# Kernel tuning notes

Measured on AMD Instinct MI355X. Metric: run time of the kernel, lower is better.

## Reference

```python
import jax, jax.numpy as jnp
import numpy as np

B, S, H, D, E = 1, 2048, 16, 64, 1024
STRIDE, LCMP = 16, 32          # compression stride / block
LSEL, TOPN = 64, 16            # selection block size / top-k blocks
WIN = 512                      # sliding window
NEG = jnp.float32(-1e9)


def setup_inputs() -> dict:
    key = jax.random.key(0)
    ks = jax.random.split(key, 5)
    q = jax.random.normal(ks[0], (B, S, H, D), jnp.float32)
    k = jax.random.normal(ks[1], (B, S, H, D), jnp.float32)
    v = jax.random.normal(ks[2], (B, S, H, D), jnp.float32)
    x = jax.random.normal(ks[3], (B, S, E), jnp.float32)
    Wg = jax.random.normal(ks[4], (E, 3), jnp.float32) * 0.02
    bg = jnp.zeros((3,), jnp.float32)
    cu_seqlens = jnp.array([0, S], jnp.int32)
    max_seqlen = S
    return {"q": q, "k": k, "v": v, "x": x, "Wg": Wg, "bg": bg,
            "cu_seqlens": cu_seqlens, "max_seqlen": max_seqlen}


def _nsa_forward(q, k, v, x, Wg, bg):
    scale = 1.0 / np.sqrt(D)
    t = jnp.arange(S)
    num_cmp = (S - LCMP) // STRIDE + 1   # 127
    num_sel = S // LSEL                  # 32

    # ---- branch 1: compressed-KV attention (mean-pooled blocks) ----
    starts = jnp.arange(num_cmp) * STRIDE
    widx = starts[:, None] + jnp.arange(LCMP)          # (num_cmp, LCMP)
    Kc = k[:, widx].mean(axis=2)                        # (B, num_cmp, H, D)
    Vc = v[:, widx].mean(axis=2)
    logits_c = jnp.einsum('bshd,bchd->bhsc', q, Kc) * scale
    # query t may attend only to fully-past compressed blocks
    mask_c = (starts + LCMP)[None, :] <= (t[:, None] + 1)   # (S, num_cmp)
    p_c = jax.nn.softmax(jnp.where(mask_c[None, None], logits_c, NEG), axis=-1)
    valid_c = mask_c.any(axis=-1).astype(q.dtype)           # (S,) zero-out empty rows
    p_c = p_c * valid_c[None, None, :, None]
    o_cmp = jnp.einsum('bhsc,bchd->bshd', p_c, Vc)

    # ---- branch 2: top-k selected-block attention ----
    # map compressed-block scores -> selection-block importance (overlap sum)
    sel_s = jnp.arange(num_sel) * LSEL
    overlap = ((starts[:, None] < sel_s[None, :] + LSEL) &
               (starts[:, None] + LCMP > sel_s[None, :])).astype(q.dtype)  # (num_cmp, num_sel)
    p_sel = jnp.einsum('bhsc,cn->bhsn', p_c, overlap)        # (B,H,S,num_sel)
    _, top_idx = jax.lax.top_k(p_sel, TOPN)                  # (B,H,S,TOPN)
    sel_blk = jax.nn.one_hot(top_idx, num_sel).sum(axis=-2) > 0   # (B,H,S,num_sel)
    own_blk = jax.nn.one_hot(t // LSEL, num_sel) > 0              # always include own block
    sel_blk = sel_blk | own_blk[None, None]
    sel_tok = jnp.repeat(sel_blk, LSEL, axis=-1)             # (B,H,S,S) token-level mask

    causal = t[:, None] >= t[None, :]                        # (S,S)
    logits = jnp.einsum('bshd,bthd->bhst', q, k) * scale     # (B,H,S,S), shared by 2 branches
    a_sel = jax.nn.softmax(jnp.where(sel_tok & causal[None, None], logits, NEG), axis=-1)
    o_sel = jnp.einsum('bhst,bthd->bshd', a_sel, v)

    # ---- branch 3: sliding-window attention ----
    win_mask = causal & (t[:, None] - t[None, :] < WIN)
    a_win = jax.nn.softmax(jnp.where(win_mask[None, None], logits, NEG), axis=-1)
    o_win = jnp.einsum('bhst,bthd->bshd', a_win, v)

    # ---- learned gating over the 3 branches ----
    g = jax.nn.sigmoid(x @ Wg + bg)                          # (B,S,3)
    out = (g[..., 0][..., None, None] * o_cmp +
           g[..., 1][..., None, None] * o_sel +
           g[..., 2][..., None, None] * o_win)
    return out                                               # (B,S,H,D)


def reference(q, k, v, x, Wg, bg, cu_seqlens, max_seqlen):
    return _nsa_forward(q, k, v, x, Wg, bg)
```

## Files before the change

### kernel.cpp

```cpp
#include <hip/hip_runtime.h>
#include <hip/hip_bf16.h>
#include <math.h>

#define H_NUM 16
#define D_DIM 64
#define S_LEN 2048
#define E_DIM 1024
#define NC    127
#define TOPN  16
#define SCALE 0.125f

typedef short s16x8 __attribute__((ext_vector_type(8)));
typedef short s16x4 __attribute__((ext_vector_type(4)));
typedef float f32x4 __attribute__((ext_vector_type(4)));
typedef unsigned short ushort_t;

__device__ __forceinline__ unsigned short f2b(float f) {
    __hip_bfloat16 h = __float2bfloat16(f);
    return *reinterpret_cast<unsigned short*>(&h);
}
__device__ __forceinline__ float b2f(unsigned short u) {
    __hip_bfloat16 h = *reinterpret_cast<__hip_bfloat16*>(&u);
    return __bfloat162float(h);
}
__device__ __forceinline__ s16x8 pack8(float4 a, float4 b) {
    s16x8 r;
    r[0] = (short)f2b(a.x); r[1] = (short)f2b(a.y);
    r[2] = (short)f2b(a.z); r[3] = (short)f2b(a.w);
    r[4] = (short)f2b(b.x); r[5] = (short)f2b(b.y);
    r[6] = (short)f2b(b.z); r[7] = (short)f2b(b.w);
    return r;
}
__device__ __forceinline__ f32x4 mfma16(s16x8 a, s16x8 b, f32x4 c) {
    return __builtin_amdgcn_mfma_f32_16x16x32_bf16(a, b, c, 0, 0, 0);
}
__device__ __forceinline__ void wave_lds_fence() {
    asm volatile("s_waitcnt lgkmcnt(0)" ::: "memory");
    __builtin_amdgcn_sched_barrier(0);
}
__device__ __forceinline__ int swP(int r, int c) { return r * 128 + (c ^ ((r & 7) << 2)); }
__device__ __forceinline__ int swB(int r, int c) { return r * 128 + (c ^ ((r & 7) << 3)); }

__device__ __forceinline__ float wave_sum(float v) {
#pragma unroll
    for (int off = 32; off; off >>= 1) v += __shfl_xor(v, off, 64);
    return v;
}

__global__ __launch_bounds__(64) void nsa_compress(
    const float* __restrict__ k, const float* __restrict__ v,
    ushort_t* __restrict__ KcHi, ushort_t* __restrict__ KcLo, ushort_t* __restrict__ VcT)
{
    int bid = blockIdx.x;
    int h = bid >> 7, c = bid & 127;
    int lane = threadIdx.x;
    float mk = 0.f, mv = 0.f;
    if (c < NC) {
        int s0 = c * 16;
#pragma unroll 4
        for (int i = 0; i < 32; ++i) {
            mk += k[((size_t)(s0 + i) * H_NUM + h) * D_DIM + lane];
            mv += v[((size_t)(s0 + i) * H_NUM + h) * D_DIM + lane];
        }
        mk *= (1.f / 32.f); mv *= (1.f / 32.f);
    }
    unsigned short khi = f2b(mk);
    KcHi[((size_t)h * 128 + c) * 64 + lane] = khi;
    KcLo[((size_t)h * 128 + c) * 64 + lane] = f2b(mk - b2f(khi));
    VcT[((size_t)h * 64 + lane) * 128 + c] = f2b(mv);
}

__global__ __launch_bounds__(256) void nsa_cast_k(
    const float* __restrict__ k, ushort_t* __restrict__ Kb)
{
    int idx = (blockIdx.x * 256 + threadIdx.x) * 4;
    int d = idx & 63, s = (idx >> 6) & 2047, h = idx >> 17;
    float4 f = *(const float4*)(k + ((size_t)s * H_NUM + h) * D_DIM + d);
    s16x4 u;
    u[0] = (short)f2b(f.x); u[1] = (short)f2b(f.y);
    u[2] = (short)f2b(f.z); u[3] = (short)f2b(f.w);
    *(s16x4*)(Kb + idx) = u;
}

__global__ __launch_bounds__(256) void nsa_cast_vt(
    const float* __restrict__ v, ushort_t* __restrict__ VtB)
{
    __shared__ ushort_t T[64][136];
    int h = blockIdx.x >> 4, s0 = (blockIdx.x & 15) << 7;
    int tid = threadIdx.x;
#pragma unroll
    for (int rep = 0; rep < 8; ++rep) {
        int idx = rep * 256 + tid;
        int i = idx >> 4, d4 = (idx & 15) << 2;
        float4 f = *(const float4*)(v + ((size_t)(s0 + i) * H_NUM + h) * D_DIM + d4);
        T[d4 + 0][i] = f2b(f.x); T[d4 + 1][i] = f2b(f.y);
        T[d4 + 2][i] = f2b(f.z); T[d4 + 3][i] = f2b(f.w);
    }
    __syncthreads();
    int d = tid >> 2, i0 = (tid & 3) << 5;
    ushort_t* dst = VtB + ((size_t)h * 64 + d) * 2048 + s0 + i0;
#pragma unroll
    for (int jj = 0; jj < 32; jj += 8)
        *(s16x8*)(dst + jj) = *(const s16x8*)&T[d][i0 + jj];
}

__global__ __launch_bounds__(64) void nsa_gate(
    const float* __restrict__ x, const float* __restrict__ Wg,
    const float* __restrict__ bg, float* __restrict__ g)
{
    int s = blockIdx.x, lane = threadIdx.x;
    float a0 = 0.f, a1 = 0.f, a2 = 0.f;
    for (int i = lane; i < E_DIM; i += 64) {
        float xv = x[(size_t)s * E_DIM + i];
        a0 = fmaf(xv, Wg[i * 3 + 0], a0);
        a1 = fmaf(xv, Wg[i * 3 + 1], a1);
        a2 = fmaf(xv, Wg[i * 3 + 2], a2);
    }
    a0 = wave_sum(a0); a1 = wave_sum(a1); a2 = wave_sum(a2);
    if (lane == 0) {
        g[s * 3 + 0] = 1.f / (1.f + expf(-(a0 + bg[0])));
        g[s * 3 + 1] = 1.f / (1.f + expf(-(a1 + bg[1])));
        g[s * 3 + 2] = 1.f / (1.f + expf(-(a2 + bg[2])));
    }
}

__global__ __launch_bounds__(256) void nsa_main(
    const float* __restrict__ q,
    const ushort_t* __restrict__ Kb, const ushort_t* __restrict__ VtB,
    const ushort_t* __restrict__ KcHi, const ushort_t* __restrict__ KcLo,
    const ushort_t* __restrict__ VcT,
    const float* __restrict__ gat, float* __restrict__ out)
{
    __shared__ __align__(16) float Pl[4 * 2048];
    __shared__ __align__(16) float psl[4 * 512];

    const int bid  = blockIdx.x;
    const int h    = bid & 15;
    const int grp  = bid >> 4;
    const int tile = (grp < 16) ? (31 - grp) : (grp - 16);
    const int t0   = tile << 6;
    const int tid  = threadIdx.x;
    const int w    = tid >> 6;
    const int lane = tid & 63;
    const int lr   = lane & 15;
    const int g    = lane >> 4;

    float*    Pw   = Pl + w * 2048;
    ushort_t* Pb   = (ushort_t*)Pw;
    float*    pslw = psl + w * 512;

    int trow[4];
#pragma unroll
    for (int r = 0; r < 4; ++r) trow[r] = t0 + 16 * w + 4 * g + r;

    s16x8 qa[2], ql[2];
    {
        const float* qrow = q + ((size_t)(t0 + 16 * w + lr) * H_NUM + h) * D_DIM;
#pragma unroll
        for (int kk = 0; kk < 2; ++kk) {
            float4 a = *(const float4*)(qrow + kk * 32 + g * 8);
            float4 b = *(const float4*)(qrow + kk * 32 + g * 8 + 4);
            s16x8 hi = pack8(a, b);
            float4 ar, br;
            ar.x = a.x - b2f((unsigned short)hi[0]); ar.y = a.y - b2f((unsigned short)hi[1]);
            ar.z = a.z - b2f((unsigned short)hi[2]); ar.w = a.w - b2f((unsigned short)hi[3]);
            br.x = b.x - b2f((unsigned short)hi[4]); br.y = b.y - b2f((unsigned short)hi[5]);
            br.z = b.z - b2f((unsigned short)hi[6]); br.w = b.w - b2f((unsigned short)hi[7]);
            qa[kk] = hi;
            ql[kk] = pack8(ar, br);
        }
    }

    f32x4 sc8[8];
#pragma unroll
    for (int ct = 0; ct < 8; ++ct) {
        f32x4 acc = {0.f, 0.f, 0.f, 0.f};
#pragma unroll
        for (int kk = 0; kk < 2; ++kk) {
            const size_t off = ((size_t)h * 128 + 16 * ct + lr) * 64 + kk * 32 + g * 8;
            s16x8 khi = *(const s16x8*)(KcHi + off);
            s16x8 klo = *(const s16x8*)(KcLo + off);
            acc = mfma16(qa[kk], khi, acc);
            acc = mfma16(ql[kk], khi, acc);
            acc = mfma16(qa[kk], klo, acc);
        }
        sc8[ct] = acc;
    }

    int nv[4];
#pragma unroll
    for (int r = 0; r < 4; ++r) nv[r] = (trow[r] >= 31) ? (((trow[r] - 31) >> 4) + 1) : 0;

    float pm[4] = {-3e38f, -3e38f, -3e38f, -3e38f};
#pragma unroll
    for (int ct = 0; ct < 8; ++ct)
#pragma unroll
        for (int r = 0; r < 4; ++r) {
            int c = 16 * ct + lr;
            float s = sc8[ct][r] * SCALE;
            if (c < nv[r]) pm[r] = fmaxf(pm[r], s);
        }
#pragma unroll
    for (int off = 8; off >= 1; off >>= 1)
#pragma unroll
        for (int r = 0; r < 4; ++r) pm[r] = fmaxf(pm[r], __shfl_xor(pm[r], off, 64));

    float l1[4] = {0.f, 0.f, 0.f, 0.f};
#pragma unroll
    for (int ct = 0; ct < 8; ++ct)
#pragma unroll
        for (int r = 0; r < 4; ++r) {
            int c = 16 * ct + lr;
            float p = (c < nv[r]) ? __expf(sc8[ct][r] * SCALE - pm[r]) : 0.f;
            l1[r] += p;
            Pw[swP(4 * g + r, 16 * ct + lr)] = p;
        }
#pragma unroll
    for (int off = 8; off >= 1; off >>= 1)
#pragma unroll
        for (int r = 0; r < 4; ++r) l1[r] += __shfl_xor(l1[r], off, 64);
    wave_lds_fence();

#pragma unroll
    for (int rep = 0; rep < 8; ++rep) {
        int item = rep * 64 + lane;
        int n = item >> 4, row = item & 15;
        int lo = 4 * n - 1; if (lo < 0) lo = 0;
        int hi = 4 * n + 3; if (hi > NC - 1) hi = NC - 1;
        float s = 0.f;
        for (int c = lo; c <= hi; ++c) s += Pw[swP(row, c)];
        pslw[n * 16 + row] = s;
    }
    wave_lds_fence();

    unsigned mymask = 0u;
    {
        float pv[32];
#pragma unroll
        for (int n = 0; n < 32; ++n) pv[n] = (lane < 16) ? pslw[n * 16 + lane] : 0.f;
        for (int it = 0; it < TOPN; ++it) {
            float best = -1.f; int bi = 0;
#pragma unroll
            for (int n = 0; n < 32; ++n) {
                float val = ((mymask >> n) & 1u) ? -2.f : pv[n];
                if (val > best) { best = val; bi = n; }
            }
            mymask |= 1u << bi;
        }
        mymask |= 1u << tile;
        if (lane >= 16) mymask = 0u;
    }
    unsigned um = mymask;
#pragma unroll
    for (int off = 32; off >= 1; off >>= 1) um |= __shfl_xor(um, off, 64);
    unsigned selreg[4];
#pragma unroll
    for (int r = 0; r < 4; ++r) selreg[r] = __shfl(mymask, 4 * g + r, 64);

    f32x4 oc[4];
#pragma unroll
    for (int dt = 0; dt < 4; ++dt) { f32x4 z = {0.f, 0.f, 0.f, 0.f}; oc[dt] = z; }
#pragma unroll
    for (int kk = 0; kk < 4; ++kk) {
        float4 a0 = *(const float4*)&Pw[swP(lr, kk * 32 + g * 8)];
        float4 a1 = *(const float4*)&Pw[swP(lr, kk * 32 + g * 8 + 4)];
        s16x8 pa = pack8(a0, a1);
#pragma unroll
        for (int dt = 0; dt < 4; ++dt)
            oc[dt] = mfma16(pa, *(const s16x8*)(VcT + ((size_t)h * 64 + 16 * dt + lr) * 128 + kk * 32 + g * 8), oc[dt]);
    }

    const int winlo = (tile >= 8) ? (tile - 8) : 0;

    float m2[4], l2[4], m3[4], l3[4];
    f32x4 o2[4], o3[4];
#pragma unroll
    for (int r = 0; r < 4; ++r) { m2[r] = -1e30f; l2[r] = 0.f; m3[r] = -1e30f; l3[r] = 0.f; }
#pragma unroll
    for (int dt = 0; dt < 4; ++dt) { f32x4 z = {0.f, 0.f, 0.f, 0.f}; o2[dt] = z; o3[dt] = z; }

    for (int n = 0; n <= tile; ++n) {
        const bool sel_on = (um >> n) & 1u;
        const bool win_on = n >= winlo;
        if (!sel_on && !win_on) continue;
        const int base = n << 6;

        f32x4 s4[4];
#pragma unroll
        for (int ct = 0; ct < 4; ++ct) {
            f32x4 acc = {0.f, 0.f, 0.f, 0.f};
#pragma unroll
            for (int kk = 0; kk < 2; ++kk)
                acc = mfma16(qa[kk],
                    *(const s16x8*)(Kb + ((size_t)h * 2048 + base + 16 * ct + lr) * 64 + kk * 32 + g * 8), acc);
            s4[ct] = acc;
        }

        if (sel_on) {
            float rm[4] = {-3e38f, -3e38f, -3e38f, -3e38f};
#pragma unroll
            for (int ct = 0; ct < 4; ++ct)
#pragma unroll
                for (int r = 0; r < 4; ++r) {
                    int j = base + 16 * ct + lr;
                    bool ok = ((selreg[r] >> n) & 1u) && (j <= trow[r]);
                    float s = s4[ct][r] * SCALE;
                    if (ok) rm[r] = fmaxf(rm[r], s);
                }
#pragma unroll
            for (int off = 8; off >= 1; off >>= 1)
#pragma unroll
                for (int r = 0; r < 4; ++r) rm[r] = fmaxf(rm[r], __shfl_xor(rm[r], off, 64));
            float al[4], rs[4] = {0.f, 0.f, 0.f, 0.f};
#pragma unroll
            for (int r = 0; r < 4; ++r) {
                float mn = fmaxf(m2[r], rm[r]);
                al[r] = __expf(m2[r] - mn);
                m2[r] = mn;
            }
#pragma unroll
            for (int ct = 0; ct < 4; ++ct)
#pragma unroll
                for (int r = 0; r < 4; ++r) {
                    int j = base + 16 * ct + lr;
                    bool ok = ((selreg[r] >> n) & 1u) && (j <= trow[r]);
                    float p = ok ? __expf(s4[ct][r] * SCALE - m2[r]) : 0.f;
                    rs[r] += p;
                    Pb[swB(4 * g + r, 16 * ct + lr)] = f2b(p);
                }
#pragma unroll
            for (int off = 8; off >= 1; off >>= 1)
#pragma unroll
                for (int r = 0; r < 4; ++r) rs[r] += __shfl_xor(rs[r], off, 64);
#pragma unroll
            for (int r = 0; r < 4; ++r) l2[r] = l2[r] * al[r] + rs[r];
#pragma unroll
            for (int dt = 0; dt < 4; ++dt)
#pragma unroll
                for (int r = 0; r < 4; ++r) o2[dt][r] *= al[r];
        }
        if (win_on) {
            float rm[4] = {-3e38f, -3e38f, -3e38f, -3e38f};
#pragma unroll
            for (int ct = 0; ct < 4; ++ct)
#pragma unroll
                for (int r = 0; r < 4; ++r) {
                    int j = base + 16 * ct + lr;
                    bool ok = (j >= trow[r] - 511) && (j <= trow[r]);
                    float s = s4[ct][r] * SCALE;
                    if (ok) rm[r] = fmaxf(rm[r], s);
                }
#pragma unroll
            for (int off = 8; off >= 1; off >>= 1)
#pragma unroll
                for (int r = 0; r < 4; ++r) rm[r] = fmaxf(rm[r], __shfl_xor(rm[r], off, 64));
            float al[4], rs[4] = {0.f, 0.f, 0.f, 0.f};
#pragma unroll
            for (int r = 0; r < 4; ++r) {
                float mn = fmaxf(m3[r], rm[r]);
                al[r] = __expf(m3[r] - mn);
                m3[r] = mn;
            }
#pragma unroll
            for (int ct = 0; ct < 4; ++ct)
#pragma unroll
                for (int r = 0; r < 4; ++r) {
                    int j = base + 16 * ct + lr;
                    bool ok = (j >= trow[r] - 511) && (j <= trow[r]);
                    float p = ok ? __expf(s4[ct][r] * SCALE - m3[r]) : 0.f;
                    rs[r] += p;
                    Pb[2048 + swB(4 * g + r, 16 * ct + lr)] = f2b(p);
                }
#pragma unroll
            for (int off = 8; off >= 1; off >>= 1)
#pragma unroll
                for (int r = 0; r < 4; ++r) rs[r] += __shfl_xor(rs[r], off, 64);
#pragma unroll
            for (int r = 0; r < 4; ++r) l3[r] = l3[r] * al[r] + rs[r];
#pragma unroll
            for (int dt = 0; dt < 4; ++dt)
#pragma unroll
                for (int r = 0; r < 4; ++r) o3[dt][r] *= al[r];
        }
        wave_lds_fence();

        if (sel_on) {
#pragma unroll
            for (int kk = 0; kk < 2; ++kk) {
                s16x8 pa = *(const s16x8*)&Pb[swB(lr, kk * 32 + g * 8)];
#pragma unroll
                for (int dt = 0; dt < 4; ++dt)
                    o2[dt] = mfma16(pa,
                        *(const s16x8*)(VtB + ((size_t)h * 64 + 16 * dt + lr) * 2048 + base + kk * 32 + g * 8), o2[dt]);
            }
        }
        if (win_on) {
#pragma unroll
            for (int kk = 0; kk < 2; ++kk) {
                s16x8 pa = *(const s16x8*)&Pb[2048 + swB(lr, kk * 32 + g * 8)];
#pragma unroll
                for (int dt = 0; dt < 4; ++dt)
                    o3[dt] = mfma16(pa,
                        *(const s16x8*)(VtB + ((size_t)h * 64 + 16 * dt + lr) * 2048 + base + kk * 32 + g * 8), o3[dt]);
            }
        }
    }

#pragma unroll
    for (int r = 0; r < 4; ++r) {
        const float* gp = gat + (size_t)trow[r] * 3;
        float g0 = gp[0], g1 = gp[1], g2 = gp[2];
        float invc = nv[r] ? (1.f / l1[r]) : 0.f;
        float i2 = 1.f / l2[r], i3 = 1.f / l3[r];
#pragma unroll
        for (int dt = 0; dt < 4; ++dt) {
            float val = g0 * (oc[dt][r] * invc) + g1 * (o2[dt][r] * i2) + g2 * (o3[dt][r] * i3);
            out[((size_t)trow[r] * H_NUM + h) * D_DIM + 16 * dt + lr] = val;
        }
    }
}

extern "C" void kernel_launch(void* const* d_in, const int* in_sizes, int n_in,
                              void* d_out, int out_size, void* d_ws, size_t ws_size,
                              hipStream_t stream) {
    const float* q  = (const float*)d_in[0];
    const float* k  = (const float*)d_in[1];
    const float* v  = (const float*)d_in[2];
    const float* x  = (const float*)d_in[3];
    const float* Wg = (const float*)d_in[4];
    const float* bg = (const float*)d_in[5];
    float* out = (float*)d_out;

    ushort_t* Kb   = (ushort_t*)d_ws;
    ushort_t* VtB  = Kb  + (size_t)16 * 2048 * 64;
    ushort_t* KcHi = VtB + (size_t)16 * 64 * 2048;
    ushort_t* KcLo = KcHi + (size_t)16 * 128 * 64;
    ushort_t* VcT  = KcLo + (size_t)16 * 128 * 64;
    float*    g    = (float*)(VcT + (size_t)16 * 64 * 128);

    nsa_compress<<<16 * 128, 64, 0, stream>>>(k, v, KcHi, KcLo, VcT);
    nsa_cast_k  <<<2048, 256, 0, stream>>>(k, Kb);
    nsa_cast_vt <<<256, 256, 0, stream>>>(v, VtB);
    nsa_gate    <<<S_LEN, 64, 0, stream>>>(x, Wg, bg, g);
    nsa_main    <<<512, 256, 0, stream>>>(q, Kb, VtB, KcHi, KcLo, VcT, g, out);
}
```

Measured before the change: 152.3 us.

## Split attention branches across paired waves with 512-thread blocks and merge results

Doubles the block to 8 waves and pairs each 16-row group across two waves. One wave computes the compressed branch and top-k selection while its partner runs the sliding-window loop. Both waves then share the selected-block loop by alternating blocks, and the partial online-softmax states are merged through shared memory. This aims to shorten the serial per-wave critical path and raise the number of resident waves, at the cost of extra LDS, two block-wide barriers and a merge step.

```diff
diff --git a/kernel.cpp b/kernel.cpp
--- a/kernel.cpp
+++ b/kernel.cpp
@@ -39,7 +39,7 @@
     __builtin_amdgcn_sched_barrier(0);
 }
 __device__ __forceinline__ int swP(int r, int c) { return r * 128 + (c ^ ((r & 7) << 2)); }
-__device__ __forceinline__ int swB(int r, int c) { return r * 128 + (c ^ ((r & 7) << 3)); }
+__device__ __forceinline__ int swU(int r, int c) { return r * 64  + (c ^ ((r & 7) << 3)); }
 
 __device__ __forceinline__ float wave_sum(float v) {
 #pragma unroll
@@ -124,15 +124,18 @@
     }
 }
 
-__global__ __launch_bounds__(256) void nsa_main(
+__global__ __launch_bounds__(512, 4) void nsa_main(
     const float* __restrict__ q,
     const ushort_t* __restrict__ Kb, const ushort_t* __restrict__ VtB,
     const ushort_t* __restrict__ KcHi, const ushort_t* __restrict__ KcLo,
     const ushort_t* __restrict__ VcT,
     const float* __restrict__ gat, float* __restrict__ out)
 {
-    __shared__ __align__(16) float Pl[4 * 2048];
-    __shared__ __align__(16) float psl[4 * 512];
+    __shared__ __align__(16) float    P1[4 * 2048];
+    __shared__ __align__(16) float    psl[4 * 512];
+    __shared__ __align__(16) ushort_t BP[4 * 2048];
+    __shared__ float    mrg[4 * 64];
+    __shared__ unsigned selm_l[64];
 
     const int bid  = blockIdx.x;
     const int h    = bid & 15;
@@ -141,21 +144,26 @@
     const int t0   = tile << 6;
     const int tid  = threadIdx.x;
     const int w    = tid >> 6;
+    const int pair = w & 3;
+    const bool isA = w < 4;
     const int lane = tid & 63;
     const int lr   = lane & 15;
     const int g    = lane >> 4;
-
-    float*    Pw   = Pl + w * 2048;
-    ushort_t* Pb   = (ushort_t*)Pw;
-    float*    pslw = psl + w * 512;
+    const int rb   = t0 + 16 * pair;
+
+    float*    P1w  = P1 + pair * 2048;
+    float*    pslw = psl + pair * 512;
+    ushort_t* APb  = (ushort_t*)pslw;
+    ushort_t* BPw  = BP + pair * 2048;
+    float*    mrgw = mrg + pair * 64;
 
     int trow[4];
 #pragma unroll
-    for (int r = 0; r < 4; ++r) trow[r] = t0 + 16 * w + 4 * g + r;
+    for (int r = 0; r < 4; ++r) trow[r] = rb + 4 * g + r;
 
     s16x8 qa[2], ql[2];
     {
-        const float* qrow = q + ((size_t)(t0 + 16 * w + lr) * H_NUM + h) * D_DIM;
+        const float* qrow = q + ((size_t)(rb + lr) * H_NUM + h) * D_DIM;
 #pragma unroll
         for (int kk = 0; kk < 2; ++kk) {
             float4 a = *(const float4*)(qrow + kk * 32 + g * 8);
@@ -171,175 +179,120 @@
         }
     }
 
-    f32x4 sc8[8];
-#pragma unroll
-    for (int ct = 0; ct < 8; ++ct) {
-        f32x4 acc = {0.f, 0.f, 0.f, 0.f};
-#pragma unroll
-        for (int kk = 0; kk < 2; ++kk) {
-            const size_t off = ((size_t)h * 128 + 16 * ct + lr) * 64 + kk * 32 + g * 8;
-            s16x8 khi = *(const s16x8*)(KcHi + off);
-            s16x8 klo = *(const s16x8*)(KcLo + off);
-            acc = mfma16(qa[kk], khi, acc);
-            acc = mfma16(ql[kk], khi, acc);
-            acc = mfma16(qa[kk], klo, acc);
-        }
-        sc8[ct] = acc;
-    }
-
     int nv[4];
 #pragma unroll
     for (int r = 0; r < 4; ++r) nv[r] = (trow[r] >= 31) ? (((trow[r] - 31) >> 4) + 1) : 0;
 
-    float pm[4] = {-3e38f, -3e38f, -3e38f, -3e38f};
-#pragma unroll
-    for (int ct = 0; ct < 8; ++ct)
-#pragma unroll
-        for (int r = 0; r < 4; ++r) {
-            int c = 16 * ct + lr;
-            float s = sc8[ct][r] * SCALE;
-            if (c < nv[r]) pm[r] = fmaxf(pm[r], s);
-        }
-#pragma unroll
-    for (int off = 8; off >= 1; off >>= 1)
-#pragma unroll
-        for (int r = 0; r < 4; ++r) pm[r] = fmaxf(pm[r], __shfl_xor(pm[r], off, 64));
-
     float l1[4] = {0.f, 0.f, 0.f, 0.f};
-#pragma unroll
-    for (int ct = 0; ct < 8; ++ct)
-#pragma unroll
-        for (int r = 0; r < 4; ++r) {
-            int c = 16 * ct + lr;
-            float p = (c < nv[r]) ? __expf(sc8[ct][r] * SCALE - pm[r]) : 0.f;
-            l1[r] += p;
-            Pw[swP(4 * g + r, 16 * ct + lr)] = p;
-        }
-#pragma unroll
-    for (int off = 8; off >= 1; off >>= 1)
-#pragma unroll
-        for (int r = 0; r < 4; ++r) l1[r] += __shfl_xor(l1[r], off, 64);
-    wave_lds_fence();
-
-#pragma unroll
-    for (int rep = 0; rep < 8; ++rep) {
-        int item = rep * 64 + lane;
-        int n = item >> 4, row = item & 15;
-        int lo = 4 * n - 1; if (lo < 0) lo = 0;
-        int hi = 4 * n + 3; if (hi > NC - 1) hi = NC - 1;
-        float s = 0.f;
-        for (int c = lo; c <= hi; ++c) s += Pw[swP(row, c)];
-        pslw[n * 16 + row] = s;
-    }
-    wave_lds_fence();
-
-    unsigned mymask = 0u;
-    {
-        float pv[32];
-#pragma unroll
-        for (int n = 0; n < 32; ++n) pv[n] = (lane < 16) ? pslw[n * 16 + lane] : 0.f;
-        for (int it = 0; it < TOPN; ++it) {
-            float best = -1.f; int bi = 0;
-#pragma unroll
-            for (int n = 0; n < 32; ++n) {
-                float val = ((mymask >> n) & 1u) ? -2.f : pv[n];
-                if (val > best) { best = val; bi = n; }
-            }
-            mymask |= 1u << bi;
-        }
-        mymask |= 1u << tile;
-        if (lane >= 16) mymask = 0u;
-    }
-    unsigned um = mymask;
-#pragma unroll
-    for (int off = 32; off >= 1; off >>= 1) um |= __shfl_xor(um, off, 64);
-    unsigned selreg[4];
-#pragma unroll
-    for (int r = 0; r < 4; ++r) selreg[r] = __shfl(mymask, 4 * g + r, 64);
-
     f32x4 oc[4];
 #pragma unroll
     for (int dt = 0; dt < 4; ++dt) { f32x4 z = {0.f, 0.f, 0.f, 0.f}; oc[dt] = z; }
-#pragma unroll
-    for (int kk = 0; kk < 4; ++kk) {
-        float4 a0 = *(const float4*)&Pw[swP(lr, kk * 32 + g * 8)];
-        float4 a1 = *(const float4*)&Pw[swP(lr, kk * 32 + g * 8 + 4)];
-        s16x8 pa = pack8(a0, a1);
-#pragma unroll
-        for (int dt = 0; dt < 4; ++dt)
-            oc[dt] = mfma16(pa, *(const s16x8*)(VcT + ((size_t)h * 64 + 16 * dt + lr) * 128 + kk * 32 + g * 8), oc[dt]);
-    }
 
     const int winlo = (tile >= 8) ? (tile - 8) : 0;
-
-    float m2[4], l2[4], m3[4], l3[4];
-    f32x4 o2[4], o3[4];
-#pragma unroll
-    for (int r = 0; r < 4; ++r) { m2[r] = -1e30f; l2[r] = 0.f; m3[r] = -1e30f; l3[r] = 0.f; }
-#pragma unroll
-    for (int dt = 0; dt < 4; ++dt) { f32x4 z = {0.f, 0.f, 0.f, 0.f}; o2[dt] = z; o3[dt] = z; }
-
-    for (int n = 0; n <= tile; ++n) {
-        const bool sel_on = (um >> n) & 1u;
-        const bool win_on = n >= winlo;
-        if (!sel_on && !win_on) continue;
-        const int base = n << 6;
-
-        f32x4 s4[4];
-#pragma unroll
-        for (int ct = 0; ct < 4; ++ct) {
+    float m3[4], l3[4];
+    f32x4 o3[4];
+#pragma unroll
+    for (int r = 0; r < 4; ++r) { m3[r] = -1e30f; l3[r] = 0.f; }
+#pragma unroll
+    for (int dt = 0; dt < 4; ++dt) { f32x4 z = {0.f, 0.f, 0.f, 0.f}; o3[dt] = z; }
+
+    if (isA) {
+        f32x4 sc8[8];
+#pragma unroll
+        for (int ct = 0; ct < 8; ++ct) {
             f32x4 acc = {0.f, 0.f, 0.f, 0.f};
 #pragma unroll
-            for (int kk = 0; kk < 2; ++kk)
-                acc = mfma16(qa[kk],
-                    *(const s16x8*)(Kb + ((size_t)h * 2048 + base + 16 * ct + lr) * 64 + kk * 32 + g * 8), acc);
-            s4[ct] = acc;
-        }
-
-        if (sel_on) {
-            float rm[4] = {-3e38f, -3e38f, -3e38f, -3e38f};
-#pragma unroll
-            for (int ct = 0; ct < 4; ++ct)
-#pragma unroll
-                for (int r = 0; r < 4; ++r) {
-                    int j = base + 16 * ct + lr;
-                    bool ok = ((selreg[r] >> n) & 1u) && (j <= trow[r]);
-                    float s = s4[ct][r] * SCALE;
-                    if (ok) rm[r] = fmaxf(rm[r], s);
+            for (int kk = 0; kk < 2; ++kk) {
+                const size_t off = ((size_t)h * 128 + 16 * ct + lr) * 64 + kk * 32 + g * 8;
+                s16x8 khi = *(const s16x8*)(KcHi + off);
+                s16x8 klo = *(const s16x8*)(KcLo + off);
+                acc = mfma16(qa[kk], khi, acc);
+                acc = mfma16(ql[kk], khi, acc);
+                acc = mfma16(qa[kk], klo, acc);
+            }
+            sc8[ct] = acc;
+        }
+
+        float pm[4] = {-3e38f, -3e38f, -3e38f, -3e38f};
+#pragma unroll
+        for (int ct = 0; ct < 8; ++ct)
+#pragma unroll
+            for (int r = 0; r < 4; ++r) {
+                int c = 16 * ct + lr;
+                float s = sc8[ct][r] * SCALE;
+                if (c < nv[r]) pm[r] = fmaxf(pm[r], s);
+            }
+#pragma unroll
+        for (int off = 8; off >= 1; off >>= 1)
+#pragma unroll
+            for (int r = 0; r < 4; ++r) pm[r] = fmaxf(pm[r], __shfl_xor(pm[r], off, 64));
+
+#pragma unroll
+        for (int ct = 0; ct < 8; ++ct)
+#pragma unroll
+            for (int r = 0; r < 4; ++r) {
+                int c = 16 * ct + lr;
+                float p = (c < nv[r]) ? __expf(sc8[ct][r] * SCALE - pm[r]) : 0.f;
+                l1[r] += p;
+                P1w[swP(4 * g + r, 16 * ct + lr)] = p;
+            }
+#pragma unroll
+        for (int off = 8; off >= 1; off >>= 1)
+#pragma unroll
+            for (int r = 0; r < 4; ++r) l1[r] += __shfl_xor(l1[r], off, 64);
+        wave_lds_fence();
+
+#pragma unroll
+        for (int rep = 0; rep < 8; ++rep) {
+            int item = rep * 64 + lane;
+            int n = item >> 4, row = item & 15;
+            int lo = 4 * n - 1; if (lo < 0) lo = 0;
+            int hi = 4 * n + 3; if (hi > NC - 1) hi = NC - 1;
+            float s = 0.f;
+            for (int c = lo; c <= hi; ++c) s += P1w[swP(row, c)];
+            pslw[n * 16 + row] = s;
+        }
+        wave_lds_fence();
+
+        unsigned mymask = 0u;
+        {
+            float pv[32];
+#pragma unroll
+            for (int n = 0; n < 32; ++n) pv[n] = (lane < 16) ? pslw[n * 16 + lane] : 0.f;
+            for (int it = 0; it < TOPN; ++it) {
+                float best = -1.f; int bi = 0;
+#pragma unroll
+                for (int n = 0; n < 32; ++n) {
+                    float val = ((mymask >> n) & 1u) ? -2.f : pv[n];
+                    if (val > best) { best = val; bi = n; }
                 }
-#pragma unroll
-            for (int off = 8; off >= 1; off >>= 1)
-#pragma unroll
-                for (int r = 0; r < 4; ++r) rm[r] = fmaxf(rm[r], __shfl_xor(rm[r], off, 64));
-            float al[4], rs[4] = {0.f, 0.f, 0.f, 0.f};
-#pragma unroll
-            for (int r = 0; r < 4; ++r) {
-                float mn = fmaxf(m2[r], rm[r]);
-                al[r] = __expf(m2[r] - mn);
-                m2[r] = mn;
-            }
-#pragma unroll
-            for (int ct = 0; ct < 4; ++ct)
-#pragma unroll
-                for (int r = 0; r < 4; ++r) {
-                    int j = base + 16 * ct + lr;
-                    bool ok = ((selreg[r] >> n) & 1u) && (j <= trow[r]);
-                    float p = ok ? __expf(s4[ct][r] * SCALE - m2[r]) : 0.f;
-                    rs[r] += p;
-                    Pb[swB(4 * g + r, 16 * ct + lr)] = f2b(p);
-                }
-#pragma unroll
-            for (int off = 8; off >= 1; off >>= 1)
-#pragma unroll
-                for (int r = 0; r < 4; ++r) rs[r] += __shfl_xor(rs[r], off, 64);
-#pragma unroll
-            for (int r = 0; r < 4; ++r) l2[r] = l2[r] * al[r] + rs[r];
+                mymask |= 1u << bi;
+            }
+        }
+        if (lane < 16) selm_l[pair * 16 + lane] = mymask | (1u << tile);
+
+#pragma unroll
+        for (int kk = 0; kk < 4; ++kk) {
+            float4 a0 = *(const float4*)&P1w[swP(lr, kk * 32 + g * 8)];
+            float4 a1 = *(const float4*)&P1w[swP(lr, kk * 32 + g * 8 + 4)];
+            s16x8 pa = pack8(a0, a1);
 #pragma unroll
             for (int dt = 0; dt < 4; ++dt)
-#pragma unroll
-                for (int r = 0; r < 4; ++r) o2[dt][r] *= al[r];
-        }
-        if (win_on) {
+                oc[dt] = mfma16(pa, *(const s16x8*)(VcT + ((size_t)h * 64 + 16 * dt + lr) * 128 + kk * 32 + g * 8), oc[dt]);
+        }
+    } else {
+        for (int n = winlo; n <= tile; ++n) {
+            const int base = n << 6;
+            f32x4 s4[4];
+#pragma unroll
+            for (int ct = 0; ct < 4; ++ct) {
+                f32x4 acc = {0.f, 0.f, 0.f, 0.f};
+#pragma unroll
+                for (int kk = 0; kk < 2; ++kk)
+                    acc = mfma16(qa[kk],
+                        *(const s16x8*)(Kb + ((size_t)h * 2048 + base + 16 * ct + lr) * 64 + kk * 32 + g * 8), acc);
+                s4[ct] = acc;
+            }
             float rm[4] = {-3e38f, -3e38f, -3e38f, -3e38f};
 #pragma unroll
             for (int ct = 0; ct < 4; ++ct)
@@ -369,7 +322,7 @@
                     bool ok = (j >= trow[r] - 511) && (j <= trow[r]);
                     float p = ok ? __expf(s4[ct][r] * SCALE - m3[r]) : 0.f;
                     rs[r] += p;
-                    Pb[2048 + swB(4 * g + r, 16 * ct + lr)] = f2b(p);
+                    BPw[swU(4 * g + r, 16 * ct + lr)] = f2b(p);
                 }
 #pragma unroll
             for (int off = 8; off >= 1; off >>= 1)
@@ -381,23 +334,10 @@
             for (int dt = 0; dt < 4; ++dt)
 #pragma unroll
                 for (int r = 0; r < 4; ++r) o3[dt][r] *= al[r];
-        }
-        wave_lds_fence();
-
-        if (sel_on) {
+            wave_lds_fence();
 #pragma unroll
             for (int kk = 0; kk < 2; ++kk) {
-                s16x8 pa = *(const s16x8*)&Pb[swB(lr, kk * 32 + g * 8)];
-#pragma unroll
-                for (int dt = 0; dt < 4; ++dt)
-                    o2[dt] = mfma16(pa,
-                        *(const s16x8*)(VtB + ((size_t)h * 64 + 16 * dt + lr) * 2048 + base + kk * 32 + g * 8), o2[dt]);
-            }
-        }
-        if (win_on) {
-#pragma unroll
-            for (int kk = 0; kk < 2; ++kk) {
-                s16x8 pa = *(const s16x8*)&Pb[2048 + swB(lr, kk * 32 + g * 8)];
+                s16x8 pa = *(const s16x8*)&BPw[swU(lr, kk * 32 + g * 8)];
 #pragma unroll
                 for (int dt = 0; dt < 4; ++dt)
                     o3[dt] = mfma16(pa,
@@ -405,17 +345,132 @@
             }
         }
     }
-
-#pragma unroll
-    for (int r = 0; r < 4; ++r) {
-        const float* gp = gat + (size_t)trow[r] * 3;
-        float g0 = gp[0], g1 = gp[1], g2 = gp[2];
-        float invc = nv[r] ? (1.f / l1[r]) : 0.f;
-        float i2 = 1.f / l2[r], i3 = 1.f / l3[r];
-#pragma unroll
-        for (int dt = 0; dt < 4; ++dt) {
-            float val = g0 * (oc[dt][r] * invc) + g1 * (o2[dt][r] * i2) + g2 * (o3[dt][r] * i3);
-            out[((size_t)trow[r] * H_NUM + h) * D_DIM + 16 * dt + lr] = val;
+    __syncthreads();
+
+    unsigned um = selm_l[pair * 16 + lr];
+#pragma unroll
+    for (int off = 8; off >= 1; off >>= 1) um |= __shfl_xor(um, off, 64);
+    unsigned selreg[4];
+#pragma unroll
+    for (int r = 0; r < 4; ++r) selreg[r] = selm_l[pair * 16 + 4 * g + r];
+
+    float m2[4], l2[4];
+    f32x4 o2[4];
+#pragma unroll
+    for (int r = 0; r < 4; ++r) { m2[r] = -1e30f; l2[r] = 0.f; }
+#pragma unroll
+    for (int dt = 0; dt < 4; ++dt) { f32x4 z = {0.f, 0.f, 0.f, 0.f}; o2[dt] = z; }
+
+    ushort_t* myP = isA ? APb : (BPw + 1024);
+    int cnt = 0;
+    for (int n = 0; n <= tile; ++n) {
+        if (!((um >> n) & 1u)) continue;
+        bool mine = ((cnt & 1) == (isA ? 0 : 1));
+        ++cnt;
+        if (!mine) continue;
+        const int base = n << 6;
+
+        f32x4 s4[4];
+#pragma unroll
+        for (int ct = 0; ct < 4; ++ct) {
+            f32x4 acc = {0.f, 0.f, 0.f, 0.f};
+#pragma unroll
+            for (int kk = 0; kk < 2; ++kk)
+                acc = mfma16(qa[kk],
+                    *(const s16x8*)(Kb + ((size_t)h * 2048 + base + 16 * ct + lr) * 64 + kk * 32 + g * 8), acc);
+            s4[ct] = acc;
+        }
+        float rm[4] = {-3e38f, -3e38f, -3e38f, -3e38f};
+#pragma unroll
+        for (int ct = 0; ct < 4; ++ct)
+#pragma unroll
+            for (int r = 0; r < 4; ++r) {
+                int j = base + 16 * ct + lr;
+                bool ok = ((selreg[r] >> n) & 1u) && (j <= trow[r]);
+                float s = s4[ct][r] * SCALE;
+                if (ok) rm[r] = fmaxf(rm[r], s);
+            }
+#pragma unroll
+        for (int off = 8; off >= 1; off >>= 1)
+#pragma unroll
+            for (int r = 0; r < 4; ++r) rm[r] = fmaxf(rm[r], __shfl_xor(rm[r], off, 64));
+        float al[4], rs[4] = {0.f, 0.f, 0.f, 0.f};
+#pragma unroll
+        for (int r = 0; r < 4; ++r) {
+            float mn = fmaxf(m2[r], rm[r]);
+            al[r] = __expf(m2[r] - mn);
+            m2[r] = mn;
+        }
+#pragma unroll
+        for (int ct = 0; ct < 4; ++ct)
+#pragma unroll
+            for (int r = 0; r < 4; ++r) {
+                int j = base + 16 * ct + lr;
+                bool ok = ((selreg[r] >> n) & 1u) && (j <= trow[r]);
+                float p = ok ? __expf(s4[ct][r] * SCALE - m2[r]) : 0.f;
+                rs[r] += p;
+                myP[swU(4 * g + r, 16 * ct + lr)] = f2b(p);
+            }
+#pragma unroll
+        for (int off = 8; off >= 1; off >>= 1)
+#pragma unroll
+            for (int r = 0; r < 4; ++r) rs[r] += __shfl_xor(rs[r], off, 64);
+#pragma unroll
+        for (int r = 0; r < 4; ++r) l2[r] = l2[r] * al[r] + rs[r];
+#pragma unroll
+        for (int dt = 0; dt < 4; ++dt)
+#pragma unroll
+            for (int r = 0; r < 4; ++r) o2[dt][r] *= al[r];
+        wave_lds_fence();
+#pragma unroll
+        for (int kk = 0; kk < 2; ++kk) {
+            s16x8 pa = *(const s16x8*)&myP[swU(lr, kk * 32 + g * 8)];
+#pragma unroll
+            for (int dt = 0; dt < 4; ++dt)
+                o2[dt] = mfma16(pa,
+                    *(const s16x8*)(VtB + ((size_t)h * 64 + 16 * dt + lr) * 2048 + base + kk * 32 + g * 8), o2[dt]);
+        }
+    }
+
+    if (!isA) {
+#pragma unroll
+        for (int dt = 0; dt < 4; ++dt)
+#pragma unroll
+            for (int r = 0; r < 4; ++r) {
+                P1w[(4 * g + r) * 64 + 16 * dt + lr] = o2[dt][r];
+                P1w[1024 + (4 * g + r) * 64 + 16 * dt + lr] = o3[dt][r];
+            }
+        if (lr == 0)
+#pragma unroll
+            for (int r = 0; r < 4; ++r) {
+                mrgw[(4 * g + r) * 4 + 0] = m2[r];
+                mrgw[(4 * g + r) * 4 + 1] = l2[r];
+                mrgw[(4 * g + r) * 4 + 2] = m3[r];
+                mrgw[(4 * g + r) * 4 + 3] = l3[r];
+            }
+    }
+    __syncthreads();
+
+    if (isA) {
+#pragma unroll
+        for (int r = 0; r < 4; ++r) {
+            const int row = 4 * g + r;
+            float m2B = mrgw[row * 4 + 0], l2B = mrgw[row * 4 + 1];
+            float m3B = mrgw[row * 4 + 2], l3B = mrgw[row * 4 + 3];
+            float m2f = fmaxf(m2[r], m2B);
+            float eA = __expf(m2[r] - m2f), eB = __expf(m2B - m2f);
+            float l2f = l2[r] * eA + l2B * eB;
+            const float* gp = gat + (size_t)trow[r] * 3;
+            float g0 = gp[0], g1 = gp[1], g2 = gp[2];
+            float invc = nv[r] ? (1.f / l1[r]) : 0.f;
+            float i2 = 1.f / l2f, i3 = 1.f / l3B;
+#pragma unroll
+            for (int dt = 0; dt < 4; ++dt) {
+                float o2f = o2[dt][r] * eA + P1w[row * 64 + 16 * dt + lr] * eB;
+                float o3f = P1w[1024 + row * 64 + 16 * dt + lr];
+                float val = g0 * (oc[dt][r] * invc) + g1 * (o2f * i2) + g2 * (o3f * i3);
+                out[((size_t)trow[r] * H_NUM + h) * D_DIM + 16 * dt + lr] = val;
+            }
         }
     }
 }
@@ -442,5 +497,5 @@
     nsa_cast_k  <<<2048, 256, 0, stream>>>(k, Kb);
     nsa_cast_vt <<<256, 256, 0, stream>>>(v, VtB);
     nsa_gate    <<<S_LEN, 64, 0, stream>>>(x, Wg, bg, g);
-    nsa_main    <<<512, 256, 0, stream>>>(q, Kb, VtB, KcHi, KcLo, VcT, g, out);
-}
+    nsa_main    <<<512, 512, 0, stream>>>(q, Kb, VtB, KcHi, KcLo, VcT, g, out);
+}
```

Measured after the change: 153.3 us. Within noise of the previous version (+0.7%).
